# Kernel optimization log

Measured on AMD Instinct MI355X. Metric: run time of the kernel, lower is better.

## Reference

```python
import jax, jax.numpy as jnp
import numpy as np

NUM_HEADS = 8
EMBED_DIM = 128
HEAD_DIM = EMBED_DIM // NUM_HEADS  # 16
NB_FEATURES = EMBED_DIM            # 128
EPS = 1e-4


def _make_projection(nb_rows, nb_cols, rng):
    # gaussian_orthogonal_random_matrix with scaling=0
    blocks = []
    for _ in range(nb_rows // nb_cols):
        q, _ = np.linalg.qr(rng.standard_normal((nb_cols, nb_cols)))
        blocks.append(q.T)
    rem = nb_rows - (nb_rows // nb_cols) * nb_cols
    if rem > 0:
        q, _ = np.linalg.qr(rng.standard_normal((nb_cols, nb_cols)))
        blocks.append(q.T[:rem])
    final = np.concatenate(blocks, axis=0)
    mult = np.linalg.norm(rng.standard_normal((nb_rows, nb_cols)), axis=1)
    return (mult[:, None] * final).astype(np.float32)


def setup_inputs() -> dict:
    key = jax.random.key(0)
    ks = jax.random.split(key, 7)
    R, C, E = 8, 2048, EMBED_DIM
    s = 1.0 / np.sqrt(E)
    x = jax.random.normal(ks[0], (R, C, E), dtype=jnp.float32)
    Wq = jax.random.uniform(ks[1], (E, E), jnp.float32, -s, s)
    bq = jax.random.uniform(ks[2], (E,), jnp.float32, -s, s)
    Wk = jax.random.uniform(ks[3], (E, E), jnp.float32, -s, s)
    bk = jax.random.uniform(ks[4], (E,), jnp.float32, -s, s)
    Wv = jax.random.uniform(ks[5], (E, E), jnp.float32, -s, s)
    bv = jax.random.uniform(ks[6], (E,), jnp.float32, -s, s)
    proj = jnp.asarray(_make_projection(NB_FEATURES, HEAD_DIM, np.random.default_rng(0)))
    return {"x": x, "Wq": Wq, "bq": bq, "Wk": Wk, "bk": bk, "Wv": Wv, "bv": bv, "proj": proj}


def _softmax_kernel(data, proj, is_query):
    # data: (R, h, n, d); proj: (F, d)
    d = data.shape[-1]
    normalizer = d ** (-0.25)
    ratio = proj.shape[0] ** (-0.5)
    data_dash = jnp.einsum('rhnd,jd->rhnj', normalizer * data, proj)  # (R,h,n,F)
    diag = jnp.sum(data * data, axis=-1, keepdims=True) * 0.5 * normalizer ** 2
    if is_query:
        m = jnp.max(data_dash, axis=-1, keepdims=True)
    else:
        m = jnp.max(data_dash, axis=(-1, -2), keepdims=True)
    return ratio * (jnp.exp(data_dash - diag - m) + EPS)


def reference(x, Wq, bq, Wk, bk, Wv, bv, proj):
    R, C, E = x.shape
    h, hd = NUM_HEADS, HEAD_DIM

    def proj_heads(W, b):
        y = jnp.einsum('rce,fe->rcf', x, W) + b
        return y.reshape(R, C, h, hd).transpose(0, 2, 1, 3)  # (R,h,C,hd)

    q = _softmax_kernel(proj_heads(Wq, bq), proj, is_query=True)   # (R,h,C,F)
    k = _softmax_kernel(proj_heads(Wk, bk), proj, is_query=False)  # (R,h,C,F)
    v = proj_heads(Wv, bv)                                          # (R,h,C,hd)

    # fold batch (R) into the feature dim: (h, C, R*F) / (h, C, R*hd)
    qf = q.transpose(1, 2, 0, 3).reshape(h, C, R * NB_FEATURES)
    kf = k.transpose(1, 2, 0, 3).reshape(h, C, R * NB_FEATURES)
    vf = v.transpose(1, 2, 0, 3).reshape(h, C, R * hd)

    k_sum = kf.sum(axis=-2)                                   # (h, D)
    D_inv = 1.0 / jnp.einsum('hnd,hd->hn', qf, k_sum)         # (h, C)
    context = jnp.einsum('hnd,hne->hde', kf, vf)              # (h, D, Ev)
    out = jnp.einsum('hde,hnd,hn->hne', context, qf, D_inv)   # (h, C, R*hd)

    out = out.reshape(h, C, R, hd).transpose(2, 1, 0, 3).reshape(R, C, E)
    attn = jnp.einsum('hqf,hkf->hqk', qf, kf)                 # (h, C, C)
    return out, attn
```

## Files before the change

### kernel.cpp

```cpp
#include <hip/hip_runtime.h>
#include <hip/hip_bf16.h>
#include <stdint.h>

typedef __bf16 bf16x8 __attribute__((ext_vector_type(8)));
typedef float  f32x4  __attribute__((ext_vector_type(4)));

#define RATIO 0.08838834764831845f
#define EPSV  1e-4f

#define GLOBAL_AS __attribute__((address_space(1)))
#define LDS_AS    __attribute__((address_space(3)))

static __device__ __forceinline__ void gload16(const void* g, void* l) {
  __builtin_amdgcn_global_load_lds((GLOBAL_AS const void*)g, (LDS_AS void*)l, 16, 0, 0);
}

static constexpr size_t OFF_XB    = 0;
static constexpr size_t OFF_WCAT  = OFF_XB    + 4194304;
static constexpr size_t OFF_MQ    = OFF_WCAT  + 98304;
static constexpr size_t OFF_MK    = OFF_MQ    + 262144;
static constexpr size_t OFF_BCAT  = OFF_MK    + 262144;
static constexpr size_t OFF_BQF   = OFF_BCAT  + 2048;
static constexpr size_t OFF_BKF   = OFF_BQF   + 4096;
static constexpr size_t OFF_Y     = OFF_BKF   + 4096;
static constexpr size_t OFF_QF    = OFF_Y     + 25165824;
static constexpr size_t OFF_KF    = OFF_QF    + 33554432;
static constexpr size_t OFF_KFT   = OFF_KF    + 33554432;
static constexpr size_t OFF_VFT   = OFF_KFT   + 33554432;
static constexpr size_t OFF_KPART = OFF_VFT   + 4194304;
static constexpr size_t OFF_KMAX  = OFF_KPART + 4096;
static constexpr size_t OFF_KSUM  = OFF_KMAX  + 256;
static constexpr size_t OFF_DINV  = OFF_KSUM  + 32768;
static constexpr size_t OFF_CTXP  = OFF_DINV  + 65536;
static constexpr size_t OFF_CTXT  = OFF_CTXP  + 16777216;
static constexpr size_t WS_NEED   = OFF_CTXT  + 2097152;

static __device__ __forceinline__ void gemm_core(
    const __hip_bfloat16* __restrict__ A, const __hip_bfloat16* __restrict__ B,
    int lda, int ldb, int K, int tm, int tn,
    __bf16* As, __bf16* Bs, f32x4 acc[4][4]) {
  const int t    = threadIdx.x;
  const int w    = t >> 6;
  const int lane = t & 63;
  const int m_off = (w >> 1) << 6;
  const int n_off = (w & 1) << 6;
  const int r0 = t >> 2;
  const int kk = (t & 3) << 3;
  char* Asb = (char*)As + (w << 10);
  char* Bsb = (char*)Bs + (w << 10);
  const int frow = lane & 15;
  const int koff = (lane >> 4) << 3;
  for (int k0 = 0; k0 < K; k0 += 32) {
    const __hip_bfloat16* Ag = A + (size_t)(tm + r0) * lda + (k0 + kk);
    const __hip_bfloat16* Bg = B + (size_t)(tn + r0) * ldb + (k0 + kk);
    gload16(Ag, Asb);
    gload16(Ag + (size_t)64 * lda, Asb + 4096);
    gload16(Bg, Bsb);
    gload16(Bg + (size_t)64 * ldb, Bsb + 4096);
    __syncthreads();
    bf16x8 af[4], bfr[4];
#pragma unroll
    for (int mi = 0; mi < 4; ++mi)
      af[mi] = *(const bf16x8*)(As + ((m_off + mi * 16 + frow) << 5) + koff);
#pragma unroll
    for (int ni = 0; ni < 4; ++ni)
      bfr[ni] = *(const bf16x8*)(Bs + ((n_off + ni * 16 + frow) << 5) + koff);
#pragma unroll
    for (int mi = 0; mi < 4; ++mi)
#pragma unroll
      for (int ni = 0; ni < 4; ++ni)
        acc[mi][ni] = __builtin_amdgcn_mfma_f32_16x16x32_bf16(af[mi], bfr[ni], acc[mi][ni], 0, 0, 0);
    __syncthreads();
  }
}

#define ZERO_ACC(acc) do {                                   \
  _Pragma("unroll") for (int a_ = 0; a_ < 4; ++a_)           \
  _Pragma("unroll") for (int b_ = 0; b_ < 4; ++b_)           \
    acc[a_][b_] = (f32x4){0.f, 0.f, 0.f, 0.f};               \
} while (0)

__global__ void k_prepwb(const float* __restrict__ Wq, const float* __restrict__ bq,
                         const float* __restrict__ Wk, const float* __restrict__ bk,
                         const float* __restrict__ Wv, const float* __restrict__ bv,
                         __hip_bfloat16* __restrict__ Wcat, float* __restrict__ bcat) {
  int i = blockIdx.x * 256 + threadIdx.x;
  if (i < 49152) {
    int mat = i >> 14, rem = i & 16383;
    const float* W = (mat == 0) ? Wq : ((mat == 1) ? Wk : Wv);
    Wcat[i] = __float2bfloat16(W[rem]);
  }
  if (i < 384) {
    int mat = i >> 7;
    const float* b = (mat == 0) ? bq : ((mat == 1) ? bk : bv);
    bcat[i] = b[i & 127];
  }
}

__global__ void k_prepM(const float* __restrict__ Wq, const float* __restrict__ bq,
                        const float* __restrict__ Wk, const float* __restrict__ bk,
                        const float* __restrict__ proj,
                        __hip_bfloat16* __restrict__ Mq, __hip_bfloat16* __restrict__ Mk,
                        float* __restrict__ bqf, float* __restrict__ bkf) {
  int i = blockIdx.x * 256 + threadIdx.x;
  if (i < 262144) {
    int which = i >> 17;
    int rem = i & 131071;
    int hj = rem >> 7, e = rem & 127;
    int hh = hj >> 7, j = hj & 127;
    const float* W = which ? Wk : Wq;
    float s = 0.f;
#pragma unroll
    for (int u = 0; u < 16; ++u) s += proj[j * 16 + u] * W[(hh * 16 + u) * 128 + e];
    if (which) Mk[rem] = __float2bfloat16(0.5f * s);
    else       Mq[rem] = __float2bfloat16(0.5f * s);
  }
  if (i < 2048) {
    int which = i >> 10;
    int hj = i & 1023, hh = hj >> 7, j = hj & 127;
    const float* b = which ? bk : bq;
    float s = 0.f;
#pragma unroll
    for (int u = 0; u < 16; ++u) s += proj[j * 16 + u] * b[hh * 16 + u];
    if (which) bkf[hj] = 0.5f * s;
    else       bqf[hj] = 0.5f * s;
  }
}

__global__ void k_convx(const float* __restrict__ x, __hip_bfloat16* __restrict__ xb) {
  int i = (blockIdx.x * 256 + threadIdx.x) * 4;
  f32x4 v = *(const f32x4*)(x + i);
#pragma unroll
  for (int j = 0; j < 4; ++j) xb[i + j] = __float2bfloat16(v[j]);
}

__global__ __launch_bounds__(256) void k_proj(
    const __hip_bfloat16* __restrict__ xb, const __hip_bfloat16* __restrict__ Wcat,
    const float* __restrict__ bcat, float* __restrict__ Y) {
  __shared__ __align__(16) __bf16 As[4096], Bs[4096];
  const int tm = blockIdx.x << 7, tn = blockIdx.y << 7;
  f32x4 acc[4][4];
  ZERO_ACC(acc);
  gemm_core(xb, Wcat, 128, 128, 128, tm, tn, As, Bs, acc);
  const int t = threadIdx.x, w = t >> 6, lane = t & 63;
  const int m_off = (w >> 1) << 6, n_off = (w & 1) << 6;
#pragma unroll
  for (int ni = 0; ni < 4; ++ni) {
    const int col = tn + n_off + ni * 16 + (lane & 15);
    const float bias = bcat[col];
#pragma unroll
    for (int mi = 0; mi < 4; ++mi)
#pragma unroll
      for (int i = 0; i < 4; ++i) {
        const int row = tm + m_off + mi * 16 + ((lane >> 4) << 2) + i;
        Y[(size_t)row * 384 + col] = acc[mi][ni][i] + bias;
      }
  }
}

__global__ void k_vft2(const float* __restrict__ Y, __hip_bfloat16* __restrict__ vfT) {
  const int cb = blockIdx.x, r = blockIdx.y, h = blockIdx.z;
  const int c0 = cb << 7;
  __shared__ float tile[16][132];
  const int t = threadIdx.x;
  const int a = t & 15, cc0 = t >> 4;
#pragma unroll
  for (int i = 0; i < 8; ++i) {
    const int cc = cc0 + (i << 4);
    tile[a][cc] = Y[(size_t)(r * 2048 + c0 + cc) * 384 + 256 + (h << 4) + a];
  }
  __syncthreads();
  const int row = t >> 4, cg = t & 15;
  bf16x8 v;
#pragma unroll
  for (int j = 0; j < 8; ++j) v[j] = (__bf16)tile[row][(cg << 3) + j];
  *(bf16x8*)(vfT + ((size_t)((h << 7) + (r << 4) + row) << 11) + c0 + (cg << 3)) = v;
}

__global__ __launch_bounds__(256) void k_dashq(
    const __hip_bfloat16* __restrict__ xb, const __hip_bfloat16* __restrict__ Mq,
    const float* __restrict__ bqf, const float* __restrict__ Y,
    __hip_bfloat16* __restrict__ qf) {
  __shared__ __align__(16) __bf16 As[4096], Bs[4096];
  __shared__ float diag_s[128];
  __shared__ float rmax_s[2][128];
  const int h = blockIdx.y;
  const int tm = blockIdx.x << 7;
  f32x4 acc[4][4];
  ZERO_ACC(acc);
  gemm_core(xb, Mq + h * 16384, 128, 128, 128, tm, 0, As, Bs, acc);
  const int t = threadIdx.x, w = t >> 6, lane = t & 63;
  const int m_off = (w >> 1) << 6, n_off = (w & 1) << 6;
  if (t < 128) {
    const float* yp = Y + (size_t)(tm + t) * 384 + h * 16;
    float s = 0.f;
#pragma unroll
    for (int u = 0; u < 16; ++u) s += yp[u] * yp[u];
    diag_s[t] = 0.125f * s;
  }
  float bia[4];
#pragma unroll
  for (int ni = 0; ni < 4; ++ni) bia[ni] = bqf[h * 128 + n_off + ni * 16 + (lane & 15)];
  float rmx[4][4];
#pragma unroll
  for (int mi = 0; mi < 4; ++mi)
#pragma unroll
    for (int i = 0; i < 4; ++i) {
      float m0 = acc[mi][0][i] + bia[0];
      m0 = fmaxf(m0, acc[mi][1][i] + bia[1]);
      m0 = fmaxf(m0, acc[mi][2][i] + bia[2]);
      m0 = fmaxf(m0, acc[mi][3][i] + bia[3]);
      rmx[mi][i] = m0;
    }
#pragma unroll
  for (int off = 1; off < 16; off <<= 1)
#pragma unroll
    for (int mi = 0; mi < 4; ++mi)
#pragma unroll
      for (int i = 0; i < 4; ++i)
        rmx[mi][i] = fmaxf(rmx[mi][i], __shfl_xor(rmx[mi][i], off));
  if ((lane & 15) == 0) {
#pragma unroll
    for (int mi = 0; mi < 4; ++mi)
#pragma unroll
      for (int i = 0; i < 4; ++i)
        rmax_s[w & 1][m_off + mi * 16 + ((lane >> 4) << 2) + i] = rmx[mi][i];
  }
  __syncthreads();
#pragma unroll
  for (int mi = 0; mi < 4; ++mi) {
#pragma unroll
    for (int i = 0; i < 4; ++i) {
      const int rl = m_off + mi * 16 + ((lane >> 4) << 2) + i;
      const int rg = tm + rl;
      const int c = rg & 2047, r = rg >> 11;
      const float md = diag_s[rl] + fmaxf(rmax_s[0][rl], rmax_s[1][rl]);
#pragma unroll
      for (int ni = 0; ni < 4; ++ni) {
        const int j = n_off + ni * 16 + (lane & 15);
        const float f = RATIO * (__expf(acc[mi][ni][i] + bia[ni] - md) + EPSV);
        qf[((size_t)((h << 11) + c) << 10) + (r << 7) + j] = __float2bfloat16(f);
      }
    }
  }
}

__global__ __launch_bounds__(256) void k_dashk_max(
    const __hip_bfloat16* __restrict__ xb, const __hip_bfloat16* __restrict__ Mk,
    const float* __restrict__ bkf, float* __restrict__ kpart) {
  __shared__ __align__(16) __bf16 As[4096], Bs[4096];
  __shared__ float wmax[4];
  const int h = blockIdx.y;
  const int tm = blockIdx.x << 7;
  f32x4 acc[4][4];
  ZERO_ACC(acc);
  gemm_core(xb, Mk + h * 16384, 128, 128, 128, tm, 0, As, Bs, acc);
  const int t = threadIdx.x, w = t >> 6, lane = t & 63;
  const int n_off = (w & 1) << 6;
  float mx = -1e30f;
#pragma unroll
  for (int ni = 0; ni < 4; ++ni) {
    const float bia = bkf[h * 128 + n_off + ni * 16 + (lane & 15)];
#pragma unroll
    for (int mi = 0; mi < 4; ++mi)
#pragma unroll
      for (int i = 0; i < 4; ++i) mx = fmaxf(mx, acc[mi][ni][i] + bia);
  }
#pragma unroll
  for (int off = 1; off < 64; off <<= 1) mx = fmaxf(mx, __shfl_xor(mx, off));
  if (lane == 0) wmax[w] = mx;
  __syncthreads();
  if (t == 0) kpart[h * 128 + blockIdx.x] = fmaxf(fmaxf(wmax[0], wmax[1]), fmaxf(wmax[2], wmax[3]));
}

__global__ void k_kmaxred(const float* __restrict__ kpart, float* __restrict__ kmax) {
  const int t = threadIdx.x;
  const int r = t >> 3, h = t & 7;
  float m = -1e30f;
  for (int i = 0; i < 16; ++i) m = fmaxf(m, kpart[h * 128 + r * 16 + i]);
  kmax[r * 8 + h] = m;
}

__global__ __launch_bounds__(256) void k_dashk_feat(
    const __hip_bfloat16* __restrict__ xb, const __hip_bfloat16* __restrict__ Mk,
    const float* __restrict__ bkf, const float* __restrict__ Y,
    const float* __restrict__ kmax,
    __hip_bfloat16* __restrict__ kf, __hip_bfloat16* __restrict__ kfT) {
  __shared__ __align__(16) __bf16 As[4096], Bs[4096];
  __shared__ float diag_s[128];
  __shared__ __align__(16) __bf16 kT[128 * 136];
  const int h = blockIdx.y;
  const int tm = blockIdx.x << 7;
  f32x4 acc[4][4];
  ZERO_ACC(acc);
  gemm_core(xb, Mk + h * 16384, 128, 128, 128, tm, 0, As, Bs, acc);
  const int t = threadIdx.x, w = t >> 6, lane = t & 63;
  const int m_off = (w >> 1) << 6, n_off = (w & 1) << 6;
  if (t < 128) {
    const float* yp = Y + (size_t)(tm + t) * 384 + 128 + h * 16;
    float s = 0.f;
#pragma unroll
    for (int u = 0; u < 16; ++u) s += yp[u] * yp[u];
    diag_s[t] = 0.125f * s;
  }
  const int r = tm >> 11;
  const int c0 = tm & 2047;
  const float m = kmax[r * 8 + h];
  float bia[4];
#pragma unroll
  for (int ni = 0; ni < 4; ++ni) bia[ni] = bkf[h * 128 + n_off + ni * 16 + (lane & 15)];
  __syncthreads();
#pragma unroll
  for (int mi = 0; mi < 4; ++mi) {
#pragma unroll
    for (int i = 0; i < 4; ++i) {
      const int rl = m_off + mi * 16 + ((lane >> 4) << 2) + i;
      const int c = c0 + rl;
      const float dm = diag_s[rl] + m;
#pragma unroll
      for (int ni = 0; ni < 4; ++ni) {
        const int j = n_off + ni * 16 + (lane & 15);
        const float f = RATIO * (__expf(acc[mi][ni][i] + bia[ni] - dm) + EPSV);
        kf[((size_t)((h << 11) + c) << 10) + (r << 7) + j] = __float2bfloat16(f);
        kT[j * 136 + rl] = (__bf16)f;
      }
    }
  }
  __syncthreads();
  const int j2 = t >> 1, half = t & 1;
  __bf16* dst = (__bf16*)kfT + (((size_t)(h << 10) + (r << 7) + j2) << 11) + c0 + (half << 6);
  const __bf16* srcr = kT + j2 * 136 + (half << 6);
#pragma unroll
  for (int q8 = 0; q8 < 8; ++q8)
    *(bf16x8*)(dst + (q8 << 3)) = *(const bf16x8*)(srcr + (q8 << 3));
}

__global__ __launch_bounds__(256) void k_ksum2(const __hip_bfloat16* __restrict__ kfT,
                                               float* __restrict__ ksum) {
  const int t = threadIdx.x, w = t >> 6, lane = t & 63;
  const int row = blockIdx.x * 4 + w;
  const __bf16* p = (const __bf16*)kfT + ((size_t)row << 11);
  float s = 0.f;
#pragma unroll
  for (int q = 0; q < 4; ++q) {
    bf16x8 v = *(const bf16x8*)(p + ((lane + (q << 6)) << 3));
#pragma unroll
    for (int j = 0; j < 8; ++j) s += (float)v[j];
  }
#pragma unroll
  for (int off = 1; off < 64; off <<= 1) s += __shfl_xor(s, off);
  if (lane == 0) ksum[row] = s;
}

__global__ __launch_bounds__(256) void k_dinv(
    const __hip_bfloat16* __restrict__ qf, const float* __restrict__ ksum,
    float* __restrict__ dinv) {
  const int t = threadIdx.x, w = t >> 6, lane = t & 63;
  const int h = blockIdx.y;
  const int c = blockIdx.x * 4 + w;
  const __bf16* qp = (const __bf16*)qf + ((size_t)((h << 11) + c) << 10);
  const float* ks = ksum + h * 1024;
  const int d0 = lane << 4;
  bf16x8 v0 = *(const bf16x8*)(qp + d0);
  bf16x8 v1 = *(const bf16x8*)(qp + d0 + 8);
  float s = 0.f;
#pragma unroll
  for (int j = 0; j < 8; ++j) s += (float)v0[j] * ks[d0 + j] + (float)v1[j] * ks[d0 + 8 + j];
#pragma unroll
  for (int off = 1; off < 64; off <<= 1) s += __shfl_xor(s, off);
  if (lane == 0) dinv[(h << 11) + c] = 1.0f / s;
}

#define SBAR() __builtin_amdgcn_s_barrier()
#define FEN()  do { asm volatile("" ::: "memory"); __builtin_amdgcn_sched_barrier(0); } while (0)
#define PRIO1() __builtin_amdgcn_s_setprio(1)
#define PRIO0() __builtin_amdgcn_s_setprio(0)

static __device__ __forceinline__ void stage_half(
    const __hip_bfloat16* __restrict__ G, int row0, int k0, char* ldstile, int half) {
  const int t = threadIdx.x;
  const int wid = t >> 6;
  const int sr = t >> 2;
  const int scol = (((t & 3) ^ ((t >> 3) & 3)) << 3);
  gload16(G + (size_t)(row0 + half * 128 + sr) * 1024 + (k0 + scol),
          ldstile + half * 8192 + (wid << 10));
}

#define LDA4(dst, buf, qm) do {                                              \
  _Pragma("unroll") for (int mi_ = 0; mi_ < 4; ++mi_)                        \
    dst[mi_] = *(const bf16x8*)((buf) + (qm) * 8192 + mi_ * 1024 + abase);   \
} while (0)
#define LDB2(dst, buf, qn) do {                                              \
  _Pragma("unroll") for (int ni_ = 0; ni_ < 2; ++ni_)                        \
    dst[ni_] = *(const bf16x8*)((buf) + (qn) * 8192 + ni_ * 1024 + bbase);   \
} while (0)
#define MFMA8(ACC, AR, BR) do {                                              \
  _Pragma("unroll") for (int mi_ = 0; mi_ < 4; ++mi_)                        \
  _Pragma("unroll") for (int ni_ = 0; ni_ < 2; ++ni_)                        \
    ACC[mi_][ni_] = __builtin_amdgcn_mfma_f32_16x16x32_bf16(                 \
        AR[mi_], BR[ni_], ACC[mi_][ni_], 0, 0, 0);                           \
} while (0)

__global__ __launch_bounds__(512, 2) void k_attn8(
    const __hip_bfloat16* __restrict__ qf, const __hip_bfloat16* __restrict__ kf,
    float* __restrict__ attn) {
  __shared__ __align__(64) char lds[65536];
  const int lid = ((blockIdx.z << 3) + blockIdx.y) * 8 + blockIdx.x;
  const int swz = ((lid & 7) << 6) + (lid >> 3);
  const int h  = swz >> 6;
  const int tm = (((swz >> 3) & 7) << 8);
  const int tn = ((swz & 7) << 8);
  const __hip_bfloat16* Ag = qf + ((size_t)h << 21);
  const __hip_bfloat16* Bg = kf + ((size_t)h << 21);

  const int t = threadIdx.x, wid = t >> 6, lane = t & 63;
  const int f = lane & 15;
  const int wr = wid >> 2, wc = wid & 3;
  const int colpart = (((lane >> 4) ^ ((lane >> 1) & 3)) << 4);
  const int abase = (wr * 64 + f) * 64 + colpart;
  const int bbase = (wc * 32 + f) * 64 + colpart;

  f32x4 acc00[4][2] = {}, acc01[4][2] = {}, acc10[4][2] = {}, acc11[4][2] = {};
  bf16x8 aR[4], bq0[2], bq1[2];

  stage_half(Ag, tm, 0, lds, 0);
  stage_half(Bg, tn, 0, lds + 32768, 0);
  stage_half(Bg, tn, 0, lds + 32768, 1);
  stage_half(Ag, tm, 0, lds, 1);
  asm volatile("s_waitcnt vmcnt(1)" ::: "memory");
  SBAR(); FEN();

  for (int kt = 0; kt < 31; ++kt) {
    const int b = kt & 1;
    char* Ab = lds + b * 16384;
    char* Bb = lds + 32768 + b * 16384;
    char* An = lds + (b ^ 1) * 16384;
    char* Bn = lds + 32768 + (b ^ 1) * 16384;
    const int nk0 = (kt + 1) << 5;
    LDA4(aR, Ab, 0); LDB2(bq0, Bb, 0); LDB2(bq1, Bb, 1);
    stage_half(Ag, tm, nk0, An, 0);
    stage_half(Bg, tn, nk0, Bn, 0);
    SBAR(); FEN();
    PRIO1(); MFMA8(acc00, aR, bq0); MFMA8(acc01, aR, bq1); PRIO0();
    asm volatile("s_waitcnt vmcnt(2)" ::: "memory");
    SBAR(); FEN();
    LDA4(aR, Ab, 1);
    stage_half(Bg, tn, nk0, Bn, 1);
    stage_half(Ag, tm, nk0, An, 1);
    SBAR(); FEN();
    PRIO1(); MFMA8(acc10, aR, bq0); MFMA8(acc11, aR, bq1); PRIO0();
    asm volatile("s_waitcnt vmcnt(1)" ::: "memory");
    SBAR(); FEN();
  }
  {
    char* Ab = lds + 16384;
    char* Bb = lds + 32768 + 16384;
    LDA4(aR, Ab, 0); LDB2(bq0, Bb, 0); LDB2(bq1, Bb, 1);
    PRIO1(); MFMA8(acc00, aR, bq0); MFMA8(acc01, aR, bq1); PRIO0();
    asm volatile("s_waitcnt vmcnt(0)" ::: "memory");
    SBAR(); FEN();
    LDA4(aR, Ab, 1);
    PRIO1(); MFMA8(acc10, aR, bq0); MFMA8(acc11, aR, bq1); PRIO0();
  }

  float* Cc = attn + ((size_t)h << 22);
  const int rbase = tm + wr * 64 + ((lane >> 4) << 2);
  const int cbase = tn + wc * 32 + f;
#pragma unroll
  for (int mi = 0; mi < 4; ++mi)
#pragma unroll
    for (int i = 0; i < 4; ++i) {
      float* r0 = Cc + ((size_t)(rbase + mi * 16 + i) << 11) + cbase;
      float* r1 = Cc + ((size_t)(rbase + 128 + mi * 16 + i) << 11) + cbase;
#pragma unroll
      for (int ni = 0; ni < 2; ++ni) {
        r0[ni * 16]       = acc00[mi][ni][i];
        r0[128 + ni * 16] = acc01[mi][ni][i];
        r1[ni * 16]       = acc10[mi][ni][i];
        r1[128 + ni * 16] = acc11[mi][ni][i];
      }
    }
}

__global__ __launch_bounds__(256) void k_ctx(
    const __hip_bfloat16* __restrict__ vfT, const __hip_bfloat16* __restrict__ kfT,
    float* __restrict__ ctxp) {
  __shared__ __align__(16) __bf16 As[4096], Bs[4096];
  const int z = blockIdx.z, h = z >> 2, kc = z & 3;
  const int tn = blockIdx.y << 7;
  f32x4 acc[4][4];
  ZERO_ACC(acc);
  gemm_core(vfT + ((size_t)h << 18) + (kc << 9), kfT + ((size_t)h << 21) + (kc << 9),
            2048, 2048, 512, 0, tn, As, Bs, acc);
  float* Cp = ctxp + ((size_t)(kc * 8 + h) << 17);
  const int t = threadIdx.x, w = t >> 6, lane = t & 63;
  const int m_off = (w >> 1) << 6, n_off = (w & 1) << 6;
#pragma unroll
  for (int mi = 0; mi < 4; ++mi)
#pragma unroll
    for (int i = 0; i < 4; ++i) {
      const int row = m_off + mi * 16 + ((lane >> 4) << 2) + i;
#pragma unroll
      for (int ni = 0; ni < 4; ++ni) {
        const int col = tn + n_off + ni * 16 + (lane & 15);
        Cp[((size_t)row << 10) + col] = acc[mi][ni][i];
      }
    }
}

__global__ void k_ctxred(const float* __restrict__ ctxp, __hip_bfloat16* __restrict__ ctxT) {
  const int i = blockIdx.x * 256 + threadIdx.x;
  const float s = ctxp[i] + ctxp[i + 1048576] + ctxp[i + 2097152] + ctxp[i + 3145728];
  ctxT[i] = __float2bfloat16(s);
}

__global__ __launch_bounds__(256) void k_out(
    const __hip_bfloat16* __restrict__ qf, const __hip_bfloat16* __restrict__ ctxT,
    const float* __restrict__ dinv, float* __restrict__ outp) {
  __shared__ __align__(16) __bf16 As[4096], Bs[4096];
  const int h = blockIdx.z;
  const int tm = blockIdx.x << 7;
  f32x4 acc[4][4];
  ZERO_ACC(acc);
  gemm_core(qf + ((size_t)h << 21), ctxT + ((size_t)h << 17), 1024, 1024, 1024, tm, 0, As, Bs, acc);
  const int t = threadIdx.x, w = t >> 6, lane = t & 63;
  const int m_off = (w >> 1) << 6, n_off = (w & 1) << 6;
#pragma unroll
  for (int mi = 0; mi < 4; ++mi)
#pragma unroll
    for (int i = 0; i < 4; ++i) {
      const int row = tm + m_off + mi * 16 + ((lane >> 4) << 2) + i;
      const float dv = dinv[(h << 11) + row];
#pragma unroll
      for (int ni = 0; ni < 4; ++ni) {
        const int col = n_off + ni * 16 + (lane & 15);
        const int rb = col >> 4, tt = col & 15;
        outp[(((size_t)(rb << 11) + row) << 7) + (h << 4) + tt] = acc[mi][ni][i] * dv;
      }
    }
}

extern "C" void kernel_launch(void* const* d_in, const int* in_sizes, int n_in,
                              void* d_out, int out_size, void* d_ws, size_t ws_size,
                              hipStream_t stream) {
  const float* x    = (const float*)d_in[0];
  const float* Wq   = (const float*)d_in[1];
  const float* bq   = (const float*)d_in[2];
  const float* Wk   = (const float*)d_in[3];
  const float* bk   = (const float*)d_in[4];
  const float* Wv   = (const float*)d_in[5];
  const float* bv   = (const float*)d_in[6];
  const float* proj = (const float*)d_in[7];
  if (ws_size < WS_NEED) return;

  char* ws = (char*)d_ws;
  __hip_bfloat16* xb   = (__hip_bfloat16*)(ws + OFF_XB);
  __hip_bfloat16* Wcat = (__hip_bfloat16*)(ws + OFF_WCAT);
  __hip_bfloat16* Mq   = (__hip_bfloat16*)(ws + OFF_MQ);
  __hip_bfloat16* Mk   = (__hip_bfloat16*)(ws + OFF_MK);
  float* bcat = (float*)(ws + OFF_BCAT);
  float* bqf  = (float*)(ws + OFF_BQF);
  float* bkf  = (float*)(ws + OFF_BKF);
  float* Y    = (float*)(ws + OFF_Y);
  __hip_bfloat16* qf  = (__hip_bfloat16*)(ws + OFF_QF);
  __hip_bfloat16* kf  = (__hip_bfloat16*)(ws + OFF_KF);
  __hip_bfloat16* kfT = (__hip_bfloat16*)(ws + OFF_KFT);
  __hip_bfloat16* vfT = (__hip_bfloat16*)(ws + OFF_VFT);
  float* kpart = (float*)(ws + OFF_KPART);
  float* kmax  = (float*)(ws + OFF_KMAX);
  float* ksum  = (float*)(ws + OFF_KSUM);
  float* dinv  = (float*)(ws + OFF_DINV);
  float* ctxp  = (float*)(ws + OFF_CTXP);
  __hip_bfloat16* ctxT = (__hip_bfloat16*)(ws + OFF_CTXT);

  float* outp = (float*)d_out;
  float* attn = (float*)d_out + 2097152;

  k_prepwb<<<dim3(192), dim3(256), 0, stream>>>(Wq, bq, Wk, bk, Wv, bv, Wcat, bcat);
  k_prepM<<<dim3(1024), dim3(256), 0, stream>>>(Wq, bq, Wk, bk, proj, Mq, Mk, bqf, bkf);
  k_convx<<<dim3(2048), dim3(256), 0, stream>>>(x, xb);
  k_proj<<<dim3(128, 3), dim3(256), 0, stream>>>(xb, Wcat, bcat, Y);
  k_vft2<<<dim3(16, 8, 8), dim3(256), 0, stream>>>(Y, vfT);
  k_dashq<<<dim3(128, 8), dim3(256), 0, stream>>>(xb, Mq, bqf, Y, qf);
  k_dashk_max<<<dim3(128, 8), dim3(256), 0, stream>>>(xb, Mk, bkf, kpart);
  k_kmaxred<<<dim3(1), dim3(64), 0, stream>>>(kpart, kmax);
  k_dashk_feat<<<dim3(128, 8), dim3(256), 0, stream>>>(xb, Mk, bkf, Y, kmax, kf, kfT);
  k_ksum2<<<dim3(2048), dim3(256), 0, stream>>>(kfT, ksum);
  k_dinv<<<dim3(512, 8), dim3(256), 0, stream>>>(qf, ksum, dinv);
  k_attn8<<<dim3(8, 8, 8), dim3(512), 0, stream>>>(qf, kf, attn);
  k_ctx<<<dim3(1, 8, 32), dim3(256), 0, stream>>>(vfT, kfT, ctxp);
  k_ctxred<<<dim3(4096), dim3(256), 0, stream>>>(ctxp, ctxT);
  k_out<<<dim3(16, 1, 8), dim3(256), 0, stream>>>(qf, ctxT, dinv, outp);
}
```

Before: 215.0 us.

## Restructure attention GEMM to 128x64 warp tiles with 64-wide K stages

The attention-score GEMM now has each wave hold a 128x64 accumulator (8x4 MFMA tiles) instead of four 64x32 quadrants, and stages 64-wide K slices across two double-buffered halves in 128 KB of dynamic LDS. The main loop runs 15 iterations instead of 31, with an interleaved load/MFMA schedule. The aim is more MFMA work per LDS fragment load and fewer barriers. The cost is much higher register pressure and LDS use, which may cap occupancy at one block per CU despite launch_bounds(512,2). Separately, the three small prep kernels are merged into one launch to cut launch overhead.

```diff
diff --git a/kernel.cpp b/kernel.cpp
--- a/kernel.cpp
+++ b/kernel.cpp
@@ -80,58 +80,58 @@
     acc[a_][b_] = (f32x4){0.f, 0.f, 0.f, 0.f};               \
 } while (0)
 
-__global__ void k_prepwb(const float* __restrict__ Wq, const float* __restrict__ bq,
-                         const float* __restrict__ Wk, const float* __restrict__ bk,
-                         const float* __restrict__ Wv, const float* __restrict__ bv,
-                         __hip_bfloat16* __restrict__ Wcat, float* __restrict__ bcat) {
-  int i = blockIdx.x * 256 + threadIdx.x;
-  if (i < 49152) {
+__global__ void k_prep(const float* __restrict__ x,
+                       const float* __restrict__ Wq, const float* __restrict__ bq,
+                       const float* __restrict__ Wk, const float* __restrict__ bk,
+                       const float* __restrict__ Wv, const float* __restrict__ bv,
+                       const float* __restrict__ proj,
+                       __hip_bfloat16* __restrict__ xb,
+                       __hip_bfloat16* __restrict__ Wcat, float* __restrict__ bcat,
+                       __hip_bfloat16* __restrict__ Mq, __hip_bfloat16* __restrict__ Mk,
+                       float* __restrict__ bqf, float* __restrict__ bkf) {
+  const int b = blockIdx.x, t = threadIdx.x;
+  {
+    int i = (b * 256 + t) * 4;
+    f32x4 v = *(const f32x4*)(x + i);
+#pragma unroll
+    for (int j = 0; j < 4; ++j) xb[i + j] = __float2bfloat16(v[j]);
+  }
+  if (b < 1024) {
+    int i = b * 256 + t;
+    {
+      int which = i >> 17;
+      int rem = i & 131071;
+      int hj = rem >> 7, e = rem & 127;
+      int hh = hj >> 7, j = hj & 127;
+      const float* W = which ? Wk : Wq;
+      float s = 0.f;
+#pragma unroll
+      for (int u = 0; u < 16; ++u) s += proj[j * 16 + u] * W[(hh * 16 + u) * 128 + e];
+      if (which) Mk[rem] = __float2bfloat16(0.5f * s);
+      else       Mq[rem] = __float2bfloat16(0.5f * s);
+    }
+    if (i < 2048) {
+      int which = i >> 10;
+      int hj = i & 1023, hh = hj >> 7, j = hj & 127;
+      const float* bb = which ? bk : bq;
+      float s = 0.f;
+#pragma unroll
+      for (int u = 0; u < 16; ++u) s += proj[j * 16 + u] * bb[hh * 16 + u];
+      if (which) bkf[hj] = 0.5f * s;
+      else       bqf[hj] = 0.5f * s;
+    }
+  }
+  if (b < 192) {
+    int i = b * 256 + t;
     int mat = i >> 14, rem = i & 16383;
     const float* W = (mat == 0) ? Wq : ((mat == 1) ? Wk : Wv);
     Wcat[i] = __float2bfloat16(W[rem]);
-  }
-  if (i < 384) {
-    int mat = i >> 7;
-    const float* b = (mat == 0) ? bq : ((mat == 1) ? bk : bv);
-    bcat[i] = b[i & 127];
-  }
-}
-
-__global__ void k_prepM(const float* __restrict__ Wq, const float* __restrict__ bq,
-                        const float* __restrict__ Wk, const float* __restrict__ bk,
-                        const float* __restrict__ proj,
-                        __hip_bfloat16* __restrict__ Mq, __hip_bfloat16* __restrict__ Mk,
-                        float* __restrict__ bqf, float* __restrict__ bkf) {
-  int i = blockIdx.x * 256 + threadIdx.x;
-  if (i < 262144) {
-    int which = i >> 17;
-    int rem = i & 131071;
-    int hj = rem >> 7, e = rem & 127;
-    int hh = hj >> 7, j = hj & 127;
-    const float* W = which ? Wk : Wq;
-    float s = 0.f;
-#pragma unroll
-    for (int u = 0; u < 16; ++u) s += proj[j * 16 + u] * W[(hh * 16 + u) * 128 + e];
-    if (which) Mk[rem] = __float2bfloat16(0.5f * s);
-    else       Mq[rem] = __float2bfloat16(0.5f * s);
-  }
-  if (i < 2048) {
-    int which = i >> 10;
-    int hj = i & 1023, hh = hj >> 7, j = hj & 127;
-    const float* b = which ? bk : bq;
-    float s = 0.f;
-#pragma unroll
-    for (int u = 0; u < 16; ++u) s += proj[j * 16 + u] * b[hh * 16 + u];
-    if (which) bkf[hj] = 0.5f * s;
-    else       bqf[hj] = 0.5f * s;
-  }
-}
-
-__global__ void k_convx(const float* __restrict__ x, __hip_bfloat16* __restrict__ xb) {
-  int i = (blockIdx.x * 256 + threadIdx.x) * 4;
-  f32x4 v = *(const f32x4*)(x + i);
-#pragma unroll
-  for (int j = 0; j < 4; ++j) xb[i + j] = __float2bfloat16(v[j]);
+    if (i < 384) {
+      int m2 = i >> 7;
+      const float* bb = (m2 == 0) ? bq : ((m2 == 1) ? bk : bv);
+      bcat[i] = bb[i & 127];
+    }
+  }
 }
 
 __global__ __launch_bounds__(256) void k_proj(
@@ -375,110 +375,121 @@
 #define FEN()  do { asm volatile("" ::: "memory"); __builtin_amdgcn_sched_barrier(0); } while (0)
 #define PRIO1() __builtin_amdgcn_s_setprio(1)
 #define PRIO0() __builtin_amdgcn_s_setprio(0)
-
-static __device__ __forceinline__ void stage_half(
-    const __hip_bfloat16* __restrict__ G, int row0, int k0, char* ldstile, int half) {
-  const int t = threadIdx.x;
-  const int wid = t >> 6;
-  const int sr = t >> 2;
-  const int scol = (((t & 3) ^ ((t >> 3) & 3)) << 3);
-  gload16(G + (size_t)(row0 + half * 128 + sr) * 1024 + (k0 + scol),
-          ldstile + half * 8192 + (wid << 10));
-}
-
-#define LDA4(dst, buf, qm) do {                                              \
-  _Pragma("unroll") for (int mi_ = 0; mi_ < 4; ++mi_)                        \
-    dst[mi_] = *(const bf16x8*)((buf) + (qm) * 8192 + mi_ * 1024 + abase);   \
-} while (0)
-#define LDB2(dst, buf, qn) do {                                              \
-  _Pragma("unroll") for (int ni_ = 0; ni_ < 2; ++ni_)                        \
-    dst[ni_] = *(const bf16x8*)((buf) + (qn) * 8192 + ni_ * 1024 + bbase);   \
-} while (0)
-#define MFMA8(ACC, AR, BR) do {                                              \
-  _Pragma("unroll") for (int mi_ = 0; mi_ < 4; ++mi_)                        \
-  _Pragma("unroll") for (int ni_ = 0; ni_ < 2; ++ni_)                        \
-    ACC[mi_][ni_] = __builtin_amdgcn_mfma_f32_16x16x32_bf16(                 \
-        AR[mi_], BR[ni_], ACC[mi_][ni_], 0, 0, 0);                           \
+#define VMW4() do { asm volatile("s_waitcnt vmcnt(4)" ::: "memory"); } while (0)
+#define VMW0() do { asm volatile("s_waitcnt vmcnt(0)" ::: "memory"); } while (0)
+
+#define MFMA16(nlo) do {                                                      \
+  _Pragma("unroll") for (int mi_ = 0; mi_ < 8; ++mi_)                         \
+  _Pragma("unroll") for (int nj_ = 0; nj_ < 2; ++nj_)                         \
+    acc[mi_][(nlo) + nj_] = __builtin_amdgcn_mfma_f32_16x16x32_bf16(          \
+        aR[mi_], bR[nj_], acc[mi_][(nlo) + nj_], 0, 0, 0);                    \
 } while (0)
 
 __global__ __launch_bounds__(512, 2) void k_attn8(
     const __hip_bfloat16* __restrict__ qf, const __hip_bfloat16* __restrict__ kf,
     float* __restrict__ attn) {
-  __shared__ __align__(64) char lds[65536];
-  const int lid = ((blockIdx.z << 3) + blockIdx.y) * 8 + blockIdx.x;
+  extern __shared__ __align__(128) char lds[];
+  const int lid = blockIdx.x;
   const int swz = ((lid & 7) << 6) + (lid >> 3);
   const int h  = swz >> 6;
-  const int tm = (((swz >> 3) & 7) << 8);
-  const int tn = ((swz & 7) << 8);
+  const int tm = ((swz >> 3) & 7) << 8;
+  const int tn = (swz & 7) << 8;
   const __hip_bfloat16* Ag = qf + ((size_t)h << 21);
   const __hip_bfloat16* Bg = kf + ((size_t)h << 21);
 
   const int t = threadIdx.x, wid = t >> 6, lane = t & 63;
   const int f = lane & 15;
   const int wr = wid >> 2, wc = wid & 3;
-  const int colpart = (((lane >> 4) ^ ((lane >> 1) & 3)) << 4);
-  const int abase = (wr * 64 + f) * 64 + colpart;
-  const int bbase = (wc * 32 + f) * 64 + colpart;
-
-  f32x4 acc00[4][2] = {}, acc01[4][2] = {}, acc10[4][2] = {}, acc11[4][2] = {};
-  bf16x8 aR[4], bq0[2], bq1[2];
-
-  stage_half(Ag, tm, 0, lds, 0);
-  stage_half(Bg, tn, 0, lds + 32768, 0);
-  stage_half(Bg, tn, 0, lds + 32768, 1);
-  stage_half(Ag, tm, 0, lds, 1);
-  asm volatile("s_waitcnt vmcnt(1)" ::: "memory");
+  const int swzg = (((lane >> 4) ^ ((f >> 1) & 3)) << 4);
+  const int aoff = ((wr << 7) + f) * 64 + swzg;
+  const int boff = 65536 + ((wc << 6) + f) * 64 + swzg;
+  const int srow = t >> 2;
+  const int scol = (((t & 3) ^ ((t >> 3) & 3)) << 3);
+  const int sdst = wid << 10;
+
+  f32x4 acc[8][4] = {};
+  bf16x8 aR[8], bR[2];
+
+  auto stageA = [&](int buf, int kh, int k0) {
+    char* d = lds + buf * 32768 + kh * 16384 + sdst;
+    const __hip_bfloat16* g = Ag + (size_t)(tm + srow) * 1024 + k0 + (kh << 5) + scol;
+    gload16(g, d);
+    gload16(g + 128 * 1024, d + 8192);
+  };
+  auto stageB = [&](int buf, int kh, int k0) {
+    char* d = lds + 65536 + buf * 32768 + kh * 16384 + sdst;
+    const __hip_bfloat16* g = Bg + (size_t)(tn + srow) * 1024 + k0 + (kh << 5) + scol;
+    gload16(g, d);
+    gload16(g + 128 * 1024, d + 8192);
+  };
+
+  stageA(0, 0, 0); stageB(0, 0, 0); stageA(0, 1, 0); stageB(0, 1, 0);
+  VMW4();
   SBAR(); FEN();
 
-  for (int kt = 0; kt < 31; ++kt) {
-    const int b = kt & 1;
-    char* Ab = lds + b * 16384;
-    char* Bb = lds + 32768 + b * 16384;
-    char* An = lds + (b ^ 1) * 16384;
-    char* Bn = lds + 32768 + (b ^ 1) * 16384;
-    const int nk0 = (kt + 1) << 5;
-    LDA4(aR, Ab, 0); LDB2(bq0, Bb, 0); LDB2(bq1, Bb, 1);
-    stage_half(Ag, tm, nk0, An, 0);
-    stage_half(Bg, tn, nk0, Bn, 0);
+  for (int kt = 0; kt < 15; ++kt) {
+    const int buf = kt & 1, nbuf = buf ^ 1;
+    const int bo = buf * 32768;
+    const int nk0 = (kt + 1) << 6;
+#pragma unroll
+    for (int mi = 0; mi < 8; ++mi) aR[mi] = *(const bf16x8*)(lds + bo + aoff + mi * 1024);
+    bR[0] = *(const bf16x8*)(lds + bo + boff);
+    bR[1] = *(const bf16x8*)(lds + bo + boff + 1024);
+    stageA(nbuf, 0, nk0);
+    PRIO1(); MFMA16(0); PRIO0();
     SBAR(); FEN();
-    PRIO1(); MFMA8(acc00, aR, bq0); MFMA8(acc01, aR, bq1); PRIO0();
-    asm volatile("s_waitcnt vmcnt(2)" ::: "memory");
+    bR[0] = *(const bf16x8*)(lds + bo + boff + 2048);
+    bR[1] = *(const bf16x8*)(lds + bo + boff + 3072);
+    stageB(nbuf, 0, nk0);
+    PRIO1(); MFMA16(2); PRIO0();
+    VMW4();
     SBAR(); FEN();
-    LDA4(aR, Ab, 1);
-    stage_half(Bg, tn, nk0, Bn, 1);
-    stage_half(Ag, tm, nk0, An, 1);
+#pragma unroll
+    for (int mi = 0; mi < 8; ++mi) aR[mi] = *(const bf16x8*)(lds + bo + 16384 + aoff + mi * 1024);
+    bR[0] = *(const bf16x8*)(lds + bo + 16384 + boff);
+    bR[1] = *(const bf16x8*)(lds + bo + 16384 + boff + 1024);
+    stageA(nbuf, 1, nk0);
+    PRIO1(); MFMA16(0); PRIO0();
     SBAR(); FEN();
-    PRIO1(); MFMA8(acc10, aR, bq0); MFMA8(acc11, aR, bq1); PRIO0();
-    asm volatile("s_waitcnt vmcnt(1)" ::: "memory");
+    bR[0] = *(const bf16x8*)(lds + bo + 16384 + boff + 2048);
+    bR[1] = *(const bf16x8*)(lds + bo + 16384 + boff + 3072);
+    stageB(nbuf, 1, nk0);
+    PRIO1(); MFMA16(2); PRIO0();
+    VMW4();
     SBAR(); FEN();
   }
   {
-    char* Ab = lds + 16384;
-    char* Bb = lds + 32768 + 16384;
-    LDA4(aR, Ab, 0); LDB2(bq0, Bb, 0); LDB2(bq1, Bb, 1);
-    PRIO1(); MFMA8(acc00, aR, bq0); MFMA8(acc01, aR, bq1); PRIO0();
-    asm volatile("s_waitcnt vmcnt(0)" ::: "memory");
+    const int bo = 32768;
+#pragma unroll
+    for (int mi = 0; mi < 8; ++mi) aR[mi] = *(const bf16x8*)(lds + bo + aoff + mi * 1024);
+    bR[0] = *(const bf16x8*)(lds + bo + boff);
+    bR[1] = *(const bf16x8*)(lds + bo + boff + 1024);
+    PRIO1(); MFMA16(0); PRIO0();
+    bR[0] = *(const bf16x8*)(lds + bo + boff + 2048);
+    bR[1] = *(const bf16x8*)(lds + bo + boff + 3072);
+    PRIO1(); MFMA16(2); PRIO0();
+    VMW0();
     SBAR(); FEN();
-    LDA4(aR, Ab, 1);
-    PRIO1(); MFMA8(acc10, aR, bq0); MFMA8(acc11, aR, bq1); PRIO0();
+#pragma unroll
+    for (int mi = 0; mi < 8; ++mi) aR[mi] = *(const bf16x8*)(lds + bo + 16384 + aoff + mi * 1024);
+    bR[0] = *(const bf16x8*)(lds + bo + 16384 + boff);
+    bR[1] = *(const bf16x8*)(lds + bo + 16384 + boff + 1024);
+    PRIO1(); MFMA16(0); PRIO0();
+    bR[0] = *(const bf16x8*)(lds + bo + 16384 + boff + 2048);
+    bR[1] = *(const bf16x8*)(lds + bo + 16384 + boff + 3072);
+    PRIO1(); MFMA16(2); PRIO0();
   }
 
   float* Cc = attn + ((size_t)h << 22);
-  const int rbase = tm + wr * 64 + ((lane >> 4) << 2);
-  const int cbase = tn + wc * 32 + f;
-#pragma unroll
-  for (int mi = 0; mi < 4; ++mi)
+  const int rbase = tm + (wr << 7) + ((lane >> 4) << 2);
+  const int cbase = tn + (wc << 6) + f;
+#pragma unroll
+  for (int mi = 0; mi < 8; ++mi)
 #pragma unroll
     for (int i = 0; i < 4; ++i) {
-      float* r0 = Cc + ((size_t)(rbase + mi * 16 + i) << 11) + cbase;
-      float* r1 = Cc + ((size_t)(rbase + 128 + mi * 16 + i) << 11) + cbase;
-#pragma unroll
-      for (int ni = 0; ni < 2; ++ni) {
-        r0[ni * 16]       = acc00[mi][ni][i];
-        r0[128 + ni * 16] = acc01[mi][ni][i];
-        r1[ni * 16]       = acc10[mi][ni][i];
-        r1[128 + ni * 16] = acc11[mi][ni][i];
-      }
+      float* rp = Cc + ((size_t)(rbase + mi * 16 + i) << 11) + cbase;
+#pragma unroll
+      for (int ni = 0; ni < 4; ++ni) rp[ni * 16] = acc[mi][ni][i];
     }
 }
 
@@ -576,9 +587,15 @@
   float* outp = (float*)d_out;
   float* attn = (float*)d_out + 2097152;
 
-  k_prepwb<<<dim3(192), dim3(256), 0, stream>>>(Wq, bq, Wk, bk, Wv, bv, Wcat, bcat);
-  k_prepM<<<dim3(1024), dim3(256), 0, stream>>>(Wq, bq, Wk, bk, proj, Mq, Mk, bqf, bkf);
-  k_convx<<<dim3(2048), dim3(256), 0, stream>>>(x, xb);
+  static int attr_done = 0;
+  if (!attr_done) {
+    (void)hipFuncSetAttribute((const void*)k_attn8,
+                              hipFuncAttributeMaxDynamicSharedMemorySize, 131072);
+    attr_done = 1;
+  }
+
+  k_prep<<<dim3(2048), dim3(256), 0, stream>>>(x, Wq, bq, Wk, bk, Wv, bv, proj,
+                                               xb, Wcat, bcat, Mq, Mk, bqf, bkf);
   k_proj<<<dim3(128, 3), dim3(256), 0, stream>>>(xb, Wcat, bcat, Y);
   k_vft2<<<dim3(16, 8, 8), dim3(256), 0, stream>>>(Y, vfT);
   k_dashq<<<dim3(128, 8), dim3(256), 0, stream>>>(xb, Mq, bqf, Y, qf);
@@ -587,7 +604,7 @@
   k_dashk_feat<<<dim3(128, 8), dim3(256), 0, stream>>>(xb, Mk, bkf, Y, kmax, kf, kfT);
   k_ksum2<<<dim3(2048), dim3(256), 0, stream>>>(kfT, ksum);
   k_dinv<<<dim3(512, 8), dim3(256), 0, stream>>>(qf, ksum, dinv);
-  k_attn8<<<dim3(8, 8, 8), dim3(512), 0, stream>>>(qf, kf, attn);
+  k_attn8<<<dim3(512), dim3(512), 131072, stream>>>(qf, kf, attn);
   k_ctx<<<dim3(1, 8, 32), dim3(256), 0, stream>>>(vfT, kfT, ctxp);
   k_ctxred<<<dim3(4096), dim3(256), 0, stream>>>(ctxp, ctxT);
   k_out<<<dim3(16, 1, 8), dim3(256), 0, stream>>>(qf, ctxT, dinv, outp);
```

Result: faster. 201.5 us (-6.3%).
